# Kernel optimization log

Hardware: AMD Instinct MI355X
Metric: run time of the kernel (lower is better)

The kernel has to match this reference:

```python
import jax, jax.numpy as jnp
import numpy as np

N = 131072

def _project(feat, x, y):
    # feat: [H, H, C]; x, y: [N] fractional pixel coords at this resolution.
    H = feat.shape[0]
    x1 = jnp.floor(x); x2 = jnp.ceil(x)
    y1 = jnp.floor(y); y2 = jnp.ceil(y)
    xi1 = jnp.clip(x1.astype(jnp.int32), 0, H - 1)
    xi2 = jnp.clip(x2.astype(jnp.int32), 0, H - 1)
    yi1 = jnp.clip(y1.astype(jnp.int32), 0, H - 1)
    yi2 = jnp.clip(y2.astype(jnp.int32), 0, H - 1)
    Q11 = feat[xi1, yi1]  # [N, C]
    Q21 = feat[xi2, yi1]
    Q12 = feat[xi1, yi2]
    Q22 = feat[xi2, yi2]
    w11 = ((x2 - x) * (y2 - y))[:, None]
    w21 = ((x - x1) * (y2 - y))[:, None]
    w12 = ((x2 - x) * (y - y1))[:, None]
    w22 = ((x - x1) * (y - y1))[:, None]
    return w11 * Q11 + w21 * Q21 + w12 * Q12 + w22 * Q22


def setup_inputs() -> dict:
    key = jax.random.key(0)
    k0, k1, k2, k3, k4 = jax.random.split(key, 5)
    coord = jax.random.normal(k0, (N, 3), dtype=jnp.float32)
    # push Z away from 0 (camera in front of mesh), as in Pixel2Mesh data
    coord = coord.at[:, 2].add(-3.0)
    feat56 = jax.random.normal(k1, (56, 56, 64), dtype=jnp.float32)
    feat28 = jax.random.normal(k2, (28, 28, 128), dtype=jnp.float32)
    feat14 = jax.random.normal(k3, (14, 14, 256), dtype=jnp.float32)
    feat7 = jax.random.normal(k4, (7, 7, 512), dtype=jnp.float32)
    return {"coord": coord, "feat56": feat56, "feat28": feat28,
            "feat14": feat14, "feat7": feat7}


def reference(coord, feat56, feat28, feat14, feat7):
    X = coord[:, 0]; Y = coord[:, 1]; Z = coord[:, 2]
    h = 250.0 * (-Y) / (-Z) + 112.0
    w = 250.0 * X / (-Z) + 112.0
    h = jnp.clip(h, 0.0, 223.0)
    w = jnp.clip(w, 0.0, 223.0)
    # note: original passes (x=h_scaled, y=w_scaled) into project in that order
    out1 = _project(feat56, h / 4.0,  w / 4.0)   # 224/56 = 4
    out2 = _project(feat28, h / 8.0,  w / 8.0)   # 224/28 = 8
    out3 = _project(feat14, h / 16.0, w / 16.0)  # 224/14 = 16
    out4 = _project(feat7,  h / 32.0, w / 32.0)  # 224/7  = 32
    return jnp.concatenate([coord, out1, out2, out3, out4], axis=1)
```

## Files before the change

### kernel.cpp

```cpp
#include <hip/hip_runtime.h>

constexpr int PPB = 16;
constexpr int GRP = 4;
constexpr int N56 = 56*56*64;
constexpr int N28 = 28*28*128;
constexpr int N14 = 14*14*256;
constexpr int N7  = 7*7*512;
constexpr int NTOT = N56 + N28 + N14 + N7;
constexpr int CONV_BLOCKS = (NTOT + 255) / 256;

typedef float    f4v __attribute__((ext_vector_type(4)));
typedef _Float16 h4v __attribute__((ext_vector_type(4)));

__global__ __launch_bounds__(256) void convert_feats_kernel(
    const float* __restrict__ f56, const float* __restrict__ f28,
    const float* __restrict__ f14, const float* __restrict__ f7,
    _Float16* __restrict__ ws)
{
    int idx = blockIdx.x * 256 + threadIdx.x;
    if (idx >= NTOT) return;
    float v;
    if (idx < N56)              v = f56[idx];
    else if (idx < N56+N28)     v = f28[idx - N56];
    else if (idx < N56+N28+N14) v = f14[idx - (N56+N28)];
    else                        v = f7[idx - (N56+N28+N14)];
    ws[idx] = (_Float16)v;
}

__global__ __launch_bounds__(256) void GraphProjection_57483842289710_kernel(
    const float* __restrict__ coord,
    const _Float16* __restrict__ ws,
    float* __restrict__ out, int n)
{
    __shared__ float lds[GRP * 963];

    const int t = threadIdx.x;
    const int ch = 4 * t;
    const _Float16* f; int C, H; float inv;
    if (ch < 64)       { f = ws + ch;                     C = 64;  H = 56; inv = 0.25f;    }
    else if (ch < 192) { f = ws + N56 + (ch - 64);        C = 128; H = 28; inv = 0.125f;   }
    else if (ch < 448) { f = ws + N56+N28 + (ch - 192);   C = 256; H = 14; inv = 0.0625f;  }
    else               { f = ws + N56+N28+N14 + (ch-448); C = 512; H = 7;  inv = 0.03125f; }

    const int p0 = blockIdx.x * PPB;

    for (int g = 0; g < PPB / GRP; ++g) {
        const int pg = p0 + g * GRP;

        #pragma unroll
        for (int k = 0; k < GRP; ++k) {
            const int p = pg + k;
            if (p >= n) break;

            const float X = coord[p * 3 + 0];
            const float Y = coord[p * 3 + 1];
            const float Z = coord[p * 3 + 2];

            const float rz = 1.0f / (-Z);
            float h = 250.0f * (-Y) * rz + 112.0f;
            float w = 250.0f * X  * rz + 112.0f;
            h = fminf(fmaxf(h, 0.0f), 223.0f);
            w = fminf(fmaxf(w, 0.0f), 223.0f);

            if (t < 240) {
                const float x = h * inv, y = w * inv;
                const float x1 = floorf(x), x2 = ceilf(x);
                const float y1 = floorf(y), y2 = ceilf(y);
                const int xi1 = min(max((int)x1, 0), H - 1);
                const int xi2 = min(max((int)x2, 0), H - 1);
                const int yi1 = min(max((int)y1, 0), H - 1);
                const int yi2 = min(max((int)y2, 0), H - 1);
                const float w11 = (x2 - x) * (y2 - y);
                const float w21 = (x - x1) * (y2 - y);
                const float w12 = (x2 - x) * (y - y1);
                const float w22 = (x - x1) * (y - y1);

                const int r1 = xi1 * H, r2 = xi2 * H;
                const h4v a = *reinterpret_cast<const h4v*>(f + (r1 + yi1) * C);
                const h4v b = *reinterpret_cast<const h4v*>(f + (r2 + yi1) * C);
                const h4v d = *reinterpret_cast<const h4v*>(f + (r1 + yi2) * C);
                const h4v e = *reinterpret_cast<const h4v*>(f + (r2 + yi2) * C);

                float* dst = lds + k * 963 + 3 + ch;
                dst[0] = w11*(float)a.x + w21*(float)b.x + w12*(float)d.x + w22*(float)e.x;
                dst[1] = w11*(float)a.y + w21*(float)b.y + w12*(float)d.y + w22*(float)e.y;
                dst[2] = w11*(float)a.z + w21*(float)b.z + w12*(float)d.z + w22*(float)e.z;
                dst[3] = w11*(float)a.w + w21*(float)b.w + w12*(float)d.w + w22*(float)e.w;
            } else if (t < 243) {
                lds[k * 963 + (t - 240)] = coord[p * 3 + (t - 240)];
            }
        }
        __syncthreads();

        {
            const f4v* __restrict__ s4 = reinterpret_cast<const f4v*>(lds);
            f4v* __restrict__ d4 = reinterpret_cast<f4v*>(out + (size_t)pg * 963);
            #pragma unroll
            for (int i = t; i < GRP * 963 / 4; i += 256)
                __builtin_nontemporal_store(s4[i], d4 + i);
        }
        __syncthreads();
    }
}

__global__ __launch_bounds__(256) void proj_f32_kernel(
    const float* __restrict__ coord,
    const float* __restrict__ f56, const float* __restrict__ f28,
    const float* __restrict__ f14, const float* __restrict__ f7,
    float* __restrict__ out, int n)
{
    const int t = threadIdx.x;
    const int ch = 4 * t;
    const float* f; int C, H; float inv;
    if (ch < 64)       { f = f56 + ch;         C = 64;  H = 56; inv = 0.25f;    }
    else if (ch < 192) { f = f28 + (ch - 64);  C = 128; H = 28; inv = 0.125f;   }
    else if (ch < 448) { f = f14 + (ch - 192); C = 256; H = 14; inv = 0.0625f;  }
    else               { f = f7  + (ch - 448); C = 512; H = 7;  inv = 0.03125f; }
    const int p0 = blockIdx.x * PPB, pend = min(p0 + PPB, n);
    #pragma unroll 2
    for (int p = p0; p < pend; ++p) {
        float* __restrict__ orow = out + (size_t)p * 963;
        const float X = coord[p*3+0], Y = coord[p*3+1], Z = coord[p*3+2];
        const float rz = 1.0f / (-Z);
        float h = 250.0f * (-Y) * rz + 112.0f;
        float w = 250.0f * X  * rz + 112.0f;
        h = fminf(fmaxf(h, 0.0f), 223.0f);
        w = fminf(fmaxf(w, 0.0f), 223.0f);
        if (t < 240) {
            const float x = h * inv, y = w * inv;
            const float x1 = floorf(x), x2 = ceilf(x);
            const float y1 = floorf(y), y2 = ceilf(y);
            const int xi1 = min(max((int)x1, 0), H - 1);
            const int xi2 = min(max((int)x2, 0), H - 1);
            const int yi1 = min(max((int)y1, 0), H - 1);
            const int yi2 = min(max((int)y2, 0), H - 1);
            const float w11 = (x2-x)*(y2-y), w21 = (x-x1)*(y2-y);
            const float w12 = (x2-x)*(y-y1), w22 = (x-x1)*(y-y1);
            const int r1 = xi1*H, r2 = xi2*H;
            const float4 a = *reinterpret_cast<const float4*>(f + (r1+yi1)*C);
            const float4 b = *reinterpret_cast<const float4*>(f + (r2+yi1)*C);
            const float4 d = *reinterpret_cast<const float4*>(f + (r1+yi2)*C);
            const float4 e = *reinterpret_cast<const float4*>(f + (r2+yi2)*C);
            f4v r;
            r.x = w11*a.x + w21*b.x + w12*d.x + w22*e.x;
            r.y = w11*a.y + w21*b.y + w12*d.y + w22*e.y;
            r.z = w11*a.z + w21*b.z + w12*d.z + w22*e.z;
            r.w = w11*a.w + w21*b.w + w12*d.w + w22*e.w;
            *reinterpret_cast<f4v*>(orow + 3 + ch) = r;
        } else if (t < 243) {
            orow[t - 240] = coord[p*3 + (t-240)];
        }
    }
}

extern "C" void kernel_launch(void* const* d_in, const int* in_sizes, int n_in,
                              void* d_out, int out_size, void* d_ws, size_t ws_size,
                              hipStream_t stream) {
    const float* coord = (const float*)d_in[0];
    const float* f56   = (const float*)d_in[1];
    const float* f28   = (const float*)d_in[2];
    const float* f14   = (const float*)d_in[3];
    const float* f7    = (const float*)d_in[4];
    float* out = (float*)d_out;

    int n = in_sizes[0] / 3;
    int grid = (n + PPB - 1) / PPB;

    if (ws_size >= (size_t)NTOT * sizeof(_Float16)) {
        _Float16* ws = (_Float16*)d_ws;
        convert_feats_kernel<<<CONV_BLOCKS, 256, 0, stream>>>(f56, f28, f14, f7, ws);
        GraphProjection_57483842289710_kernel<<<grid, 256, 0, stream>>>(coord, ws, out, n);
    } else {
        proj_f32_kernel<<<grid, 256, 0, stream>>>(coord, f56, f28, f14, f7, out, n);
    }
}
```

Baseline: 131.6 us.

## Map one wavefront per point, drop block barriers, scalarize gather offsets

Restructures the fp16 projection kernel so each 64-lane wavefront handles one point, with each lane gathering four channel groups across the four feature levels. The per-point corner offsets go through readfirstlane so they become scalar registers, and the __syncthreads barriers are replaced by a wave-local LDS wait. Each wave then writes its own 963-float output row, with scalar head and tail stores for alignment and 16-byte nontemporal stores for the middle. This is meant to remove block-level synchronisation and the idle lanes of the old 256-thread layout, at the cost of more branchy per-lane code and four times as many blocks.

```diff
diff --git a/kernel.cpp b/kernel.cpp
--- a/kernel.cpp
+++ b/kernel.cpp
@@ -1,7 +1,5 @@
 #include <hip/hip_runtime.h>
 
-constexpr int PPB = 16;
-constexpr int GRP = 4;
 constexpr int N56 = 56*56*64;
 constexpr int N28 = 28*28*128;
 constexpr int N14 = 14*14*256;
@@ -32,74 +30,102 @@
     const _Float16* __restrict__ ws,
     float* __restrict__ out, int n)
 {
-    __shared__ float lds[GRP * 963];
-
-    const int t = threadIdx.x;
-    const int ch = 4 * t;
-    const _Float16* f; int C, H; float inv;
-    if (ch < 64)       { f = ws + ch;                     C = 64;  H = 56; inv = 0.25f;    }
-    else if (ch < 192) { f = ws + N56 + (ch - 64);        C = 128; H = 28; inv = 0.125f;   }
-    else if (ch < 448) { f = ws + N56+N28 + (ch - 192);   C = 256; H = 14; inv = 0.0625f;  }
-    else               { f = ws + N56+N28+N14 + (ch-448); C = 512; H = 7;  inv = 0.03125f; }
-
-    const int p0 = blockIdx.x * PPB;
-
-    for (int g = 0; g < PPB / GRP; ++g) {
-        const int pg = p0 + g * GRP;
-
-        #pragma unroll
-        for (int k = 0; k < GRP; ++k) {
-            const int p = pg + k;
-            if (p >= n) break;
-
-            const float X = coord[p * 3 + 0];
-            const float Y = coord[p * 3 + 1];
-            const float Z = coord[p * 3 + 2];
-
-            const float rz = 1.0f / (-Z);
-            float h = 250.0f * (-Y) * rz + 112.0f;
-            float w = 250.0f * X  * rz + 112.0f;
-            h = fminf(fmaxf(h, 0.0f), 223.0f);
-            w = fminf(fmaxf(w, 0.0f), 223.0f);
-
-            if (t < 240) {
-                const float x = h * inv, y = w * inv;
-                const float x1 = floorf(x), x2 = ceilf(x);
-                const float y1 = floorf(y), y2 = ceilf(y);
-                const int xi1 = min(max((int)x1, 0), H - 1);
-                const int xi2 = min(max((int)x2, 0), H - 1);
-                const int yi1 = min(max((int)y1, 0), H - 1);
-                const int yi2 = min(max((int)y2, 0), H - 1);
-                const float w11 = (x2 - x) * (y2 - y);
-                const float w21 = (x - x1) * (y2 - y);
-                const float w12 = (x2 - x) * (y - y1);
-                const float w22 = (x - x1) * (y - y1);
-
-                const int r1 = xi1 * H, r2 = xi2 * H;
-                const h4v a = *reinterpret_cast<const h4v*>(f + (r1 + yi1) * C);
-                const h4v b = *reinterpret_cast<const h4v*>(f + (r2 + yi1) * C);
-                const h4v d = *reinterpret_cast<const h4v*>(f + (r1 + yi2) * C);
-                const h4v e = *reinterpret_cast<const h4v*>(f + (r2 + yi2) * C);
-
-                float* dst = lds + k * 963 + 3 + ch;
-                dst[0] = w11*(float)a.x + w21*(float)b.x + w12*(float)d.x + w22*(float)e.x;
-                dst[1] = w11*(float)a.y + w21*(float)b.y + w12*(float)d.y + w22*(float)e.y;
-                dst[2] = w11*(float)a.z + w21*(float)b.z + w12*(float)d.z + w22*(float)e.z;
-                dst[3] = w11*(float)a.w + w21*(float)b.w + w12*(float)d.w + w22*(float)e.w;
-            } else if (t < 243) {
-                lds[k * 963 + (t - 240)] = coord[p * 3 + (t - 240)];
-            }
+    __shared__ float lds[4 * 963];
+    const int wave = threadIdx.x >> 6;
+    const int lane = threadIdx.x & 63;
+    const int p = blockIdx.x * 4 + wave;
+    if (p >= n) return;
+    float* __restrict__ myrow = lds + wave * 963;
+
+    const float X = coord[p * 3 + 0];
+    const float Y = coord[p * 3 + 1];
+    const float Z = coord[p * 3 + 2];
+    const float rz = 1.0f / (-Z);
+    float h = 250.0f * (-Y) * rz + 112.0f;
+    float w = 250.0f * X  * rz + 112.0f;
+    h = fminf(fmaxf(h, 0.0f), 223.0f);
+    w = fminf(fmaxf(w, 0.0f), 223.0f);
+
+#define SETUP(L, INV, HH, CC)                                                  \
+    int L##o11, L##o21, L##o12, L##o22;                                        \
+    float L##w11, L##w21, L##w12, L##w22;                                      \
+    {                                                                          \
+        const float x = h * (INV), y = w * (INV);                              \
+        const float x1 = floorf(x), x2 = ceilf(x);                             \
+        const float y1 = floorf(y), y2 = ceilf(y);                             \
+        const int xi1 = min(max((int)x1, 0), (HH) - 1);                        \
+        const int xi2 = min(max((int)x2, 0), (HH) - 1);                        \
+        const int yi1 = min(max((int)y1, 0), (HH) - 1);                        \
+        const int yi2 = min(max((int)y2, 0), (HH) - 1);                        \
+        L##o11 = __builtin_amdgcn_readfirstlane((xi1 * (HH) + yi1) * (CC));    \
+        L##o21 = __builtin_amdgcn_readfirstlane((xi2 * (HH) + yi1) * (CC));    \
+        L##o12 = __builtin_amdgcn_readfirstlane((xi1 * (HH) + yi2) * (CC));    \
+        L##o22 = __builtin_amdgcn_readfirstlane((xi2 * (HH) + yi2) * (CC));    \
+        L##w11 = (x2 - x) * (y2 - y);                                          \
+        L##w21 = (x - x1) * (y2 - y);                                          \
+        L##w12 = (x2 - x) * (y - y1);                                          \
+        L##w22 = (x - x1) * (y - y1);                                          \
+    }
+    SETUP(l0, 0.25f,    56, 64)
+    SETUP(l1, 0.125f,   28, 128)
+    SETUP(l2, 0.0625f,  14, 256)
+    SETUP(l3, 0.03125f,  7, 512)
+
+#define GATHER(L, FB, CH, DCH)                                                 \
+    {                                                                          \
+        const _Float16* fp = (FB) + (DCH);                                     \
+        const h4v a = *reinterpret_cast<const h4v*>(fp + L##o11);              \
+        const h4v b = *reinterpret_cast<const h4v*>(fp + L##o21);              \
+        const h4v d = *reinterpret_cast<const h4v*>(fp + L##o12);              \
+        const h4v e = *reinterpret_cast<const h4v*>(fp + L##o22);              \
+        float* dst = myrow + 3 + (CH);                                         \
+        dst[0] = L##w11*(float)a.x + L##w21*(float)b.x + L##w12*(float)d.x + L##w22*(float)e.x; \
+        dst[1] = L##w11*(float)a.y + L##w21*(float)b.y + L##w12*(float)d.y + L##w22*(float)e.y; \
+        dst[2] = L##w11*(float)a.z + L##w21*(float)b.z + L##w12*(float)d.z + L##w22*(float)e.z; \
+        dst[3] = L##w11*(float)a.w + L##w21*(float)b.w + L##w12*(float)d.w + L##w22*(float)e.w; \
+    }
+
+    {
+        const int q = lane, ch = 4 * q;
+        if (q < 16)      GATHER(l0, ws,             ch, ch)
+        else if (q < 48) GATHER(l1, ws + N56,       ch, ch - 64)
+        else             GATHER(l2, ws + N56 + N28, ch, ch - 192)
+    }
+    {
+        const int q = 64 + lane, ch = 4 * q;
+        if (q < 112) GATHER(l2, ws + N56 + N28,       ch, ch - 192)
+        else         GATHER(l3, ws + N56 + N28 + N14, ch, ch - 448)
+    }
+    {
+        const int q = 128 + lane, ch = 4 * q;
+        GATHER(l3, ws + N56 + N28 + N14, ch, ch - 448)
+    }
+    {
+        const int q = 192 + lane, ch = 4 * q;
+        if (q < 240) GATHER(l3, ws + N56 + N28 + N14, ch, ch - 448)
+    }
+    if (lane < 3) myrow[lane] = coord[p * 3 + lane];
+
+    asm volatile("s_waitcnt lgkmcnt(0)" ::: "memory");
+    __builtin_amdgcn_sched_barrier(0);
+
+    const size_t s = (size_t)p * 963;
+    const int k0 = p & 3;
+    if (lane < k0)
+        __builtin_nontemporal_store(myrow[lane], out + s + lane);
+    #pragma unroll
+    for (int j = 0; j < 4; ++j) {
+        const int i = lane + 64 * j;
+        if (i < 240) {
+            const float* src = myrow + k0 + 4 * i;
+            f4v v; v.x = src[0]; v.y = src[1]; v.z = src[2]; v.w = src[3];
+            __builtin_nontemporal_store(v,
+                reinterpret_cast<f4v*>(out + s + k0 + 4 * i));
         }
-        __syncthreads();
-
-        {
-            const f4v* __restrict__ s4 = reinterpret_cast<const f4v*>(lds);
-            f4v* __restrict__ d4 = reinterpret_cast<f4v*>(out + (size_t)pg * 963);
-            #pragma unroll
-            for (int i = t; i < GRP * 963 / 4; i += 256)
-                __builtin_nontemporal_store(s4[i], d4 + i);
-        }
-        __syncthreads();
+    }
+    if (lane < 3 - k0) {
+        const int idx = k0 + 960 + lane;
+        __builtin_nontemporal_store(myrow[idx], out + s + idx);
     }
 }
 
@@ -116,7 +142,7 @@
     else if (ch < 192) { f = f28 + (ch - 64);  C = 128; H = 28; inv = 0.125f;   }
     else if (ch < 448) { f = f14 + (ch - 192); C = 256; H = 14; inv = 0.0625f;  }
     else               { f = f7  + (ch - 448); C = 512; H = 7;  inv = 0.03125f; }
-    const int p0 = blockIdx.x * PPB, pend = min(p0 + PPB, n);
+    const int p0 = blockIdx.x * 16, pend = min(p0 + 16, n);
     #pragma unroll 2
     for (int p = p0; p < pend; ++p) {
         float* __restrict__ orow = out + (size_t)p * 963;
@@ -164,13 +190,14 @@
     float* out = (float*)d_out;
 
     int n = in_sizes[0] / 3;
-    int grid = (n + PPB - 1) / PPB;
 
     if (ws_size >= (size_t)NTOT * sizeof(_Float16)) {
         _Float16* ws = (_Float16*)d_ws;
         convert_feats_kernel<<<CONV_BLOCKS, 256, 0, stream>>>(f56, f28, f14, f7, ws);
+        int grid = (n + 3) / 4;
         GraphProjection_57483842289710_kernel<<<grid, 256, 0, stream>>>(coord, ws, out, n);
     } else {
+        int grid = (n + 15) / 16;
         proj_f32_kernel<<<grid, 256, 0, stream>>>(coord, f56, f28, f14, f7, out, n);
     }
 }
```

Result: slower. 139.0 us (+5.6%).
